# Kernel optimization log

Measured on AMD Instinct MI355X. Metric: run time of the kernel, lower is better.

## Reference

```python
import jax, jax.numpy as jnp
import numpy as np

D = 64  # d_model
NEG_INF = -1e9


def setup_inputs() -> dict:
    key = jax.random.key(0)
    ks = jax.random.split(key, 16)
    B, N = 16, 2048
    x = jax.random.normal(ks[0], (B, N, D), dtype=jnp.float32)
    adj = jax.random.randint(ks[1], (B, N, N), 0, 2, dtype=jnp.int32)
    s = 1.0 / np.sqrt(D)
    def lin(k, fan_in, fan_out):
        kw, kb = jax.random.split(k)
        W = jax.random.uniform(kw, (fan_in, fan_out), jnp.float32, -s, s)
        b = jax.random.uniform(kb, (fan_out,), jnp.float32, -s, s)
        return W, b
    Wq, bq = lin(ks[2], D, D)
    Wk, bk = lin(ks[3], D, D)
    Wv, bv = lin(ks[4], D, D)
    Wo, bo = lin(ks[5], D, D)
    sl = 1.0 / np.sqrt(2 * D)
    kw, kb = jax.random.split(ks[6])
    Wl = jax.random.uniform(kw, (2 * D, D), jnp.float32, -sl, sl)
    bl = jax.random.uniform(kb, (D,), jnp.float32, -sl, sl)
    return {"x": x, "adj": adj, "Wq": Wq, "bq": bq, "Wk": Wk, "bk": bk,
            "Wv": Wv, "bv": bv, "Wo": Wo, "bo": bo, "Wl": Wl, "bl": bl}


def reference(x, adj, Wq, bq, Wk, bk, Wv, bv, Wo, bo, Wl, bl):
    # single-head scaled dot-product attention masked by adjacency
    q = x @ Wq + bq          # [B,N,D]
    k = x @ Wk + bk          # [B,N,D]
    v = x @ Wv + bv          # [B,N,D]
    scores = jnp.einsum('bnd,bmd->bnm', q, k) / jnp.sqrt(jnp.float32(D))
    scores = jnp.where(adj > 0, scores, jnp.float32(NEG_INF))
    attn = jax.nn.softmax(scores, axis=-1)       # [B,N,N] graph-masked dist
    ctx = jnp.einsum('bnm,bmd->bnd', attn, v)
    ctx = ctx @ Wo + bo
    # concat residual input with attention output, project, ReLU
    y = jax.nn.relu(jnp.concatenate([x, ctx], axis=-1) @ Wl + bl)
    return (y, attn)
```

## Files before the change

### kernel.cpp

```cpp
#include <hip/hip_runtime.h>
#include <hip/hip_bf16.h>


#define NB 16
#define NN 2048
#define DI 64

using s8v  = __attribute__((ext_vector_type(8))) short;
using f32x4 = __attribute__((ext_vector_type(4))) float;

__device__ __forceinline__ ushort f2bf(float f) {
    __hip_bfloat16 h = __float2bfloat16(f);
    return *reinterpret_cast<ushort*>(&h);
}
__device__ __forceinline__ float bf2f(ushort u) {
    union { uint32_t u; float f; } v; v.u = ((uint32_t)u) << 16;
    return v.f;
}

__global__ __launch_bounds__(256)
void qkv_kernel(const float* __restrict__ x,
                const float* __restrict__ Wq, const float* __restrict__ bq,
                const float* __restrict__ Wk, const float* __restrict__ bk,
                const float* __restrict__ Wv, const float* __restrict__ bv,
                ushort* __restrict__ qh, ushort* __restrict__ ql,
                ushort* __restrict__ kh, ushort* __restrict__ kl,
                ushort* __restrict__ vt)
{
    __shared__ float xs[32 * 65];
    const int t  = threadIdx.x;
    const int r0 = blockIdx.x * 32;
    for (int idx = t; idx < 2048; idx += 256)
        xs[(idx >> 6) * 65 + (idx & 63)] = x[(size_t)r0 * 64 + idx];
    __syncthreads();

    const int col = t & 63;
    const int rg  = (t >> 6) * 8;

    float vacc[8];
    {
        float acc[8];
        #pragma unroll
        for (int i = 0; i < 8; ++i) acc[i] = bq[col];
        for (int d = 0; d < 64; ++d) {
            float w = Wq[d * 64 + col];
            #pragma unroll
            for (int i = 0; i < 8; ++i) acc[i] = fmaf(xs[(rg + i) * 65 + d], w, acc[i]);
        }
        #pragma unroll
        for (int i = 0; i < 8; ++i) {
            size_t o = (size_t)(r0 + rg + i) * 64 + col;
            ushort h = f2bf(acc[i]);
            qh[o] = h;
            ql[o] = f2bf(acc[i] - bf2f(h));
        }
    }
    {
        float acc[8];
        #pragma unroll
        for (int i = 0; i < 8; ++i) acc[i] = bk[col];
        for (int d = 0; d < 64; ++d) {
            float w = Wk[d * 64 + col];
            #pragma unroll
            for (int i = 0; i < 8; ++i) acc[i] = fmaf(xs[(rg + i) * 65 + d], w, acc[i]);
        }
        #pragma unroll
        for (int i = 0; i < 8; ++i) {
            size_t o = (size_t)(r0 + rg + i) * 64 + col;
            ushort h = f2bf(acc[i]);
            kh[o] = h;
            kl[o] = f2bf(acc[i] - bf2f(h));
        }
    }
    {
        #pragma unroll
        for (int i = 0; i < 8; ++i) vacc[i] = bv[col];
        for (int d = 0; d < 64; ++d) {
            float w = Wv[d * 64 + col];
            #pragma unroll
            for (int i = 0; i < 8; ++i) vacc[i] = fmaf(xs[(rg + i) * 65 + d], w, vacc[i]);
        }
    }
    __syncthreads();
    #pragma unroll
    for (int i = 0; i < 8; ++i) xs[(rg + i) * 65 + col] = vacc[i];
    __syncthreads();
    const int bb = r0 >> 11;
    const int n0 = r0 & 2047;
    for (int idx = t; idx < 2048; idx += 256) {
        int d = idx >> 5, j = idx & 31;
        vt[((size_t)bb * 64 + d) * 2048 + n0 + j] = f2bf(xs[j * 65 + d]);
    }
}

#define SP 2052

__global__ __launch_bounds__(512, 2)
void attn_kernel(const ushort* __restrict__ qh, const ushort* __restrict__ ql,
                 const ushort* __restrict__ kh, const ushort* __restrict__ kl,
                 const ushort* __restrict__ vt, const int* __restrict__ adj,
                 const float* __restrict__ x,
                 const float* __restrict__ Wo, const float* __restrict__ bo,
                 const float* __restrict__ Wl, const float* __restrict__ bl,
                 float* __restrict__ y, float* __restrict__ attn)
{
    __shared__ float S[16 * SP];
    __shared__ float red[512];
    __shared__ float mrow[16];
    __shared__ float rZ[16];
    __shared__ float cA[16][66];
    __shared__ float cB[16][66];
    __shared__ float cto[16][66];
    __shared__ float xs[16][64];

    const int t    = threadIdx.x;
    const int lane = t & 63;
    const int wave = t >> 6;
    const int b    = blockIdx.y;
    const int row0 = blockIdx.x * 16;

    const int la = lane & 15;
    const int ak = (lane >> 4) * 8;
    const int rb2 = (lane >> 4) * 4;

    const size_t qoff = ((size_t)(b * NN + row0) + la) * 64 + ak;
    const s8v aqh0 = *(const s8v*)(qh + qoff);
    const s8v aqh1 = *(const s8v*)(qh + qoff + 32);
    const s8v aql0 = *(const s8v*)(ql + qoff);
    const s8v aql1 = *(const s8v*)(ql + qoff + 32);

    const ushort* kph = kh + (size_t)b * NN * 64;
    const ushort* kpl = kl + (size_t)b * NN * 64;
    const int*    ap  = adj + ((size_t)b * NN + row0) * NN;

    for (int tile = 0; tile < 16; ++tile) {
        const int c = wave * 256 + tile * 16;
        const size_t ko = (size_t)(c + la) * 64 + ak;
        const s8v bh0 = *(const s8v*)(kph + ko);
        const s8v bh1 = *(const s8v*)(kph + ko + 32);
        const s8v bl0 = *(const s8v*)(kpl + ko);
        const s8v bl1 = *(const s8v*)(kpl + ko + 32);
        f32x4 acc = {0.f, 0.f, 0.f, 0.f};
        acc = __builtin_amdgcn_mfma_f32_16x16x32_bf16(aqh0, bh0, acc, 0, 0, 0);
        acc = __builtin_amdgcn_mfma_f32_16x16x32_bf16(aqh1, bh1, acc, 0, 0, 0);
        acc = __builtin_amdgcn_mfma_f32_16x16x32_bf16(aql0, bh0, acc, 0, 0, 0);
        acc = __builtin_amdgcn_mfma_f32_16x16x32_bf16(aql1, bh1, acc, 0, 0, 0);
        acc = __builtin_amdgcn_mfma_f32_16x16x32_bf16(aqh0, bl0, acc, 0, 0, 0);
        acc = __builtin_amdgcn_mfma_f32_16x16x32_bf16(aqh1, bl1, acc, 0, 0, 0);
        const int ccol = c + la;
        #pragma unroll
        for (int r = 0; r < 4; ++r) {
            int av = ap[(rb2 + r) * NN + ccol];
            S[(rb2 + r) * SP + ccol] = (av > 0) ? acc[r] * 0.125f : -1e9f;
        }
    }
    {
        const float* xp = x + (size_t)(b * NN + row0) * 64;
        for (int i2 = t; i2 < 1024; i2 += 512) xs[i2 >> 6][i2 & 63] = xp[i2];
    }
    __syncthreads();

    {
        const int r = t >> 5, i = t & 31;
        float m = -3.0e38f;
        for (int c2 = i; c2 < NN; c2 += 32) m = fmaxf(m, S[r * SP + c2]);
        red[t] = m;
        __syncthreads();
        if (t < 16) {
            float mm = red[t * 32];
            for (int j = 1; j < 32; ++j) mm = fmaxf(mm, red[t * 32 + j]);
            mrow[t] = mm;
        }
        __syncthreads();
        const float mm = mrow[r];
        float sum = 0.f;
        for (int c2 = i; c2 < NN; c2 += 32) {
            float e = __expf(S[r * SP + c2] - mm);
            S[r * SP + c2] = e;
            sum += e;
        }
        red[t] = sum;
        __syncthreads();
        if (t < 16) {
            float z = 0.f;
            for (int j = 0; j < 32; ++j) z += red[t * 32 + j];
            rZ[t] = 1.0f / z;
        }
        __syncthreads();
    }

    {
        float* aop = attn + ((size_t)b * NN + row0) * NN;
        for (int r = 0; r < 16; ++r) {
            const float rz = rZ[r];
            for (int c2 = t; c2 < NN; c2 += 512)
                aop[(size_t)r * NN + c2] = S[r * SP + c2] * rz;
        }
    }

    {
        const int half = wave >> 2;
        const int dt = (wave & 3) * 16;
        const ushort* vrow = vt + ((size_t)b * 64 + dt + la) * NN;
        f32x4 acc = {0.f, 0.f, 0.f, 0.f};
        const int kk0 = half * 1024;
        for (int kk = kk0; kk < kk0 + 1024; kk += 32) {
            const float* sp = &S[la * SP + kk + ak];
            s8v a;
            #pragma unroll
            for (int j = 0; j < 8; ++j) a[j] = (short)f2bf(sp[j]);
            const s8v bv8 = *(const s8v*)(vrow + kk + ak);
            acc = __builtin_amdgcn_mfma_f32_16x16x32_bf16(a, bv8, acc, 0, 0, 0);
        }
        float (*cbuf)[66] = half ? cB : cA;
        #pragma unroll
        for (int r = 0; r < 4; ++r) cbuf[rb2 + r][dt + la] = acc[r];
    }
    __syncthreads();

    for (int idx = t; idx < 1024; idx += 512) {
        const int r = idx >> 6, cg = idx & 63;
        const float rz = rZ[r];
        float a2 = bo[cg];
        for (int d = 0; d < 64; ++d) {
            float cv = (cA[r][d] + cB[r][d]) * rz;
            a2 = fmaf(cv, Wo[d * 64 + cg], a2);
        }
        cto[r][cg] = a2;
    }
    __syncthreads();

    {
        float* yp = y + (size_t)(b * NN + row0) * 64;
        for (int idx = t; idx < 1024; idx += 512) {
            const int r = idx >> 6, cg = idx & 63;
            float a2 = bl[cg];
            for (int d = 0; d < 64; ++d) a2 = fmaf(xs[r][d], Wl[d * 64 + cg], a2);
            for (int d = 0; d < 64; ++d) a2 = fmaf(cto[r][d], Wl[(64 + d) * 64 + cg], a2);
            yp[(size_t)r * 64 + cg] = fmaxf(a2, 0.f);
        }
    }
}

extern "C" void kernel_launch(void* const* d_in, const int* in_sizes, int n_in,
                              void* d_out, int out_size, void* d_ws, size_t ws_size,
                              hipStream_t stream) {
    const float* x  = (const float*)d_in[0];
    const int*   adj = (const int*)d_in[1];
    const float* Wq = (const float*)d_in[2];
    const float* bq = (const float*)d_in[3];
    const float* Wk = (const float*)d_in[4];
    const float* bk = (const float*)d_in[5];
    const float* Wv = (const float*)d_in[6];
    const float* bv = (const float*)d_in[7];
    const float* Wo = (const float*)d_in[8];
    const float* bo = (const float*)d_in[9];
    const float* Wl = (const float*)d_in[10];
    const float* bl = (const float*)d_in[11];

    float* y    = (float*)d_out;
    float* attn = (float*)d_out + (size_t)NB * NN * DI;

    const size_t QSZ = (size_t)NB * NN * DI;
    ushort* qh = (ushort*)d_ws;
    ushort* ql = qh + QSZ;
    ushort* kh = ql + QSZ;
    ushort* kl = kh + QSZ;
    ushort* vt = kl + QSZ;

    qkv_kernel<<<1024, 256, 0, stream>>>(x, Wq, bq, Wk, bk, Wv, bv, qh, ql, kh, kl, vt);
    attn_kernel<<<dim3(NN / 16, NB), 512, 0, stream>>>(qh, ql, kh, kl, vt, adj, x,
                                                       Wo, bo, Wl, bl, y, attn);
}
```

Measured before the change: 744.8 us.

## Keep masked scores in registers, store bf16 probabilities in LDS, remap blocks

The score tiles now stay in registers. Max and sum reductions are done with wave shuffles plus a small cross-wave buffer, which replaces the LDS-based row reductions. Exponentials are stored once as bf16 in shared memory, which halves LDS use, removes the float-to-bf16 conversion in the PV loop and allows vectorized attn writes. The grid is flattened and remapped so concurrent blocks span batches, and the x tile is read from global memory instead of being staged. The attn output is now rounded through bf16 before normalization, which adds precision error.

Result: faster. 709.7 us (-4.7%).

```diff
diff --git a/kernel.cpp b/kernel.cpp
--- a/kernel.cpp
+++ b/kernel.cpp
@@ -6,7 +6,7 @@
 #define NN 2048
 #define DI 64
 
-using s8v  = __attribute__((ext_vector_type(8))) short;
+using s8v   = __attribute__((ext_vector_type(8))) short;
 using f32x4 = __attribute__((ext_vector_type(4))) float;
 
 __device__ __forceinline__ ushort f2bf(float f) {
@@ -93,9 +93,9 @@
     }
 }
 
-#define SP 2052
-
-__global__ __launch_bounds__(512, 2)
+#define SP2 2056
+
+__global__ __launch_bounds__(512)
 void attn_kernel(const ushort* __restrict__ qh, const ushort* __restrict__ ql,
                  const ushort* __restrict__ kh, const ushort* __restrict__ kl,
                  const ushort* __restrict__ vt, const int* __restrict__ adj,
@@ -104,23 +104,26 @@
                  const float* __restrict__ Wl, const float* __restrict__ bl,
                  float* __restrict__ y, float* __restrict__ attn)
 {
-    __shared__ float S[16 * SP];
-    __shared__ float red[512];
-    __shared__ float mrow[16];
-    __shared__ float rZ[16];
+    __shared__ ushort S16[16 * SP2];
     __shared__ float cA[16][66];
     __shared__ float cB[16][66];
     __shared__ float cto[16][66];
-    __shared__ float xs[16][64];
+    __shared__ float mbuf[8][16];
+    __shared__ float zbuf[8][16];
+    __shared__ float mrow[16];
+    __shared__ float rZ[16];
 
     const int t    = threadIdx.x;
     const int lane = t & 63;
     const int wave = t >> 6;
-    const int b    = blockIdx.y;
-    const int row0 = blockIdx.x * 16;
-
-    const int la = lane & 15;
-    const int ak = (lane >> 4) * 8;
+
+    const int bid = blockIdx.x;
+    const int i0  = bid >> 3;
+    const int b   = (bid & 7) + 8 * (i0 >> 7);
+    const int row0 = (i0 & 127) * 16;
+
+    const int la  = lane & 15;
+    const int ak  = (lane >> 4) * 8;
     const int rb2 = (lane >> 4) * 4;
 
     const size_t qoff = ((size_t)(b * NN + row0) + la) * 64 + ak;
@@ -133,88 +136,120 @@
     const ushort* kpl = kl + (size_t)b * NN * 64;
     const int*    ap  = adj + ((size_t)b * NN + row0) * NN;
 
+    f32x4 acc[16];
+    int   adjv[16][4];
+    #pragma unroll
     for (int tile = 0; tile < 16; ++tile) {
         const int c = wave * 256 + tile * 16;
+        #pragma unroll
+        for (int r = 0; r < 4; ++r) adjv[tile][r] = ap[(rb2 + r) * NN + c + la];
         const size_t ko = (size_t)(c + la) * 64 + ak;
         const s8v bh0 = *(const s8v*)(kph + ko);
         const s8v bh1 = *(const s8v*)(kph + ko + 32);
         const s8v bl0 = *(const s8v*)(kpl + ko);
         const s8v bl1 = *(const s8v*)(kpl + ko + 32);
-        f32x4 acc = {0.f, 0.f, 0.f, 0.f};
-        acc = __builtin_amdgcn_mfma_f32_16x16x32_bf16(aqh0, bh0, acc, 0, 0, 0);
-        acc = __builtin_amdgcn_mfma_f32_16x16x32_bf16(aqh1, bh1, acc, 0, 0, 0);
-        acc = __builtin_amdgcn_mfma_f32_16x16x32_bf16(aql0, bh0, acc, 0, 0, 0);
-        acc = __builtin_amdgcn_mfma_f32_16x16x32_bf16(aql1, bh1, acc, 0, 0, 0);
-        acc = __builtin_amdgcn_mfma_f32_16x16x32_bf16(aqh0, bl0, acc, 0, 0, 0);
-        acc = __builtin_amdgcn_mfma_f32_16x16x32_bf16(aqh1, bl1, acc, 0, 0, 0);
-        const int ccol = c + la;
+        f32x4 a = {0.f, 0.f, 0.f, 0.f};
+        a = __builtin_amdgcn_mfma_f32_16x16x32_bf16(aqh0, bh0, a, 0, 0, 0);
+        a = __builtin_amdgcn_mfma_f32_16x16x32_bf16(aqh1, bh1, a, 0, 0, 0);
+        a = __builtin_amdgcn_mfma_f32_16x16x32_bf16(aql0, bh0, a, 0, 0, 0);
+        a = __builtin_amdgcn_mfma_f32_16x16x32_bf16(aql1, bh1, a, 0, 0, 0);
+        a = __builtin_amdgcn_mfma_f32_16x16x32_bf16(aqh0, bl0, a, 0, 0, 0);
+        a = __builtin_amdgcn_mfma_f32_16x16x32_bf16(aqh1, bl1, a, 0, 0, 0);
+        acc[tile] = a;
+    }
+    #pragma unroll
+    for (int tile = 0; tile < 16; ++tile) {
+        #pragma unroll
+        for (int r = 0; r < 4; ++r)
+            acc[tile][r] = (adjv[tile][r] > 0) ? acc[tile][r] * 0.125f : -1e9f;
+    }
+
+    float vm[4];
+    #pragma unroll
+    for (int r = 0; r < 4; ++r) {
+        float m = acc[0][r];
+        #pragma unroll
+        for (int tile = 1; tile < 16; ++tile) m = fmaxf(m, acc[tile][r]);
+        vm[r] = m;
+    }
+    #pragma unroll
+    for (int off = 1; off < 16; off <<= 1) {
+        #pragma unroll
+        for (int r = 0; r < 4; ++r) vm[r] = fmaxf(vm[r], __shfl_xor(vm[r], off));
+    }
+    if (la == 0) {
+        #pragma unroll
+        for (int r = 0; r < 4; ++r) mbuf[wave][rb2 + r] = vm[r];
+    }
+    __syncthreads();
+    if (t < 16) {
+        float m = mbuf[0][t];
+        #pragma unroll
+        for (int w = 1; w < 8; ++w) m = fmaxf(m, mbuf[w][t]);
+        mrow[t] = m;
+    }
+    __syncthreads();
+
+    float gm[4], vs[4];
+    #pragma unroll
+    for (int r = 0; r < 4; ++r) { gm[r] = mrow[rb2 + r]; vs[r] = 0.f; }
+    #pragma unroll
+    for (int tile = 0; tile < 16; ++tile) {
+        const int c = wave * 256 + tile * 16;
         #pragma unroll
         for (int r = 0; r < 4; ++r) {
-            int av = ap[(rb2 + r) * NN + ccol];
-            S[(rb2 + r) * SP + ccol] = (av > 0) ? acc[r] * 0.125f : -1e9f;
-        }
-    }
-    {
-        const float* xp = x + (size_t)(b * NN + row0) * 64;
-        for (int i2 = t; i2 < 1024; i2 += 512) xs[i2 >> 6][i2 & 63] = xp[i2];
-    }
-    __syncthreads();
-
-    {
-        const int r = t >> 5, i = t & 31;
-        float m = -3.0e38f;
-        for (int c2 = i; c2 < NN; c2 += 32) m = fmaxf(m, S[r * SP + c2]);
-        red[t] = m;
-        __syncthreads();
-        if (t < 16) {
-            float mm = red[t * 32];
-            for (int j = 1; j < 32; ++j) mm = fmaxf(mm, red[t * 32 + j]);
-            mrow[t] = mm;
-        }
-        __syncthreads();
-        const float mm = mrow[r];
-        float sum = 0.f;
-        for (int c2 = i; c2 < NN; c2 += 32) {
-            float e = __expf(S[r * SP + c2] - mm);
-            S[r * SP + c2] = e;
-            sum += e;
-        }
-        red[t] = sum;
-        __syncthreads();
-        if (t < 16) {
-            float z = 0.f;
-            for (int j = 0; j < 32; ++j) z += red[t * 32 + j];
-            rZ[t] = 1.0f / z;
-        }
-        __syncthreads();
-    }
+            float e = __expf(acc[tile][r] - gm[r]);
+            vs[r] += e;
+            S16[(rb2 + r) * SP2 + c + la] = f2bf(e);
+        }
+    }
+    #pragma unroll
+    for (int off = 1; off < 16; off <<= 1) {
+        #pragma unroll
+        for (int r = 0; r < 4; ++r) vs[r] += __shfl_xor(vs[r], off);
+    }
+    if (la == 0) {
+        #pragma unroll
+        for (int r = 0; r < 4; ++r) zbuf[wave][rb2 + r] = vs[r];
+    }
+    __syncthreads();
+    if (t < 16) {
+        float z = 0.f;
+        #pragma unroll
+        for (int w = 0; w < 8; ++w) z += zbuf[w][t];
+        rZ[t] = 1.0f / z;
+    }
+    __syncthreads();
 
     {
         float* aop = attn + ((size_t)b * NN + row0) * NN;
         for (int r = 0; r < 16; ++r) {
             const float rz = rZ[r];
-            for (int c2 = t; c2 < NN; c2 += 512)
-                aop[(size_t)r * NN + c2] = S[r * SP + c2] * rz;
+            const uint2 u = *(const uint2*)(&S16[r * SP2 + 4 * t]);
+            float4 o;
+            o.x = bf2f((ushort)(u.x))       * rz;
+            o.y = bf2f((ushort)(u.x >> 16)) * rz;
+            o.z = bf2f((ushort)(u.y))       * rz;
+            o.w = bf2f((ushort)(u.y >> 16)) * rz;
+            *(float4*)(aop + (size_t)r * NN + 4 * t) = o;
         }
     }
 
     {
         const int half = wave >> 2;
-        const int dt = (wave & 3) * 16;
+        const int dt   = (wave & 3) * 16;
         const ushort* vrow = vt + ((size_t)b * 64 + dt + la) * NN;
-        f32x4 acc = {0.f, 0.f, 0.f, 0.f};
+        f32x4 a = {0.f, 0.f, 0.f, 0.f};
         const int kk0 = half * 1024;
+        #pragma unroll 4
         for (int kk = kk0; kk < kk0 + 1024; kk += 32) {
-            const float* sp = &S[la * SP + kk + ak];
-            s8v a;
-            #pragma unroll
-            for (int j = 0; j < 8; ++j) a[j] = (short)f2bf(sp[j]);
+            const s8v pa  = *(const s8v*)(&S16[la * SP2 + kk + ak]);
             const s8v bv8 = *(const s8v*)(vrow + kk + ak);
-            acc = __builtin_amdgcn_mfma_f32_16x16x32_bf16(a, bv8, acc, 0, 0, 0);
+            a = __builtin_amdgcn_mfma_f32_16x16x32_bf16(pa, bv8, a, 0, 0, 0);
         }
         float (*cbuf)[66] = half ? cB : cA;
         #pragma unroll
-        for (int r = 0; r < 4; ++r) cbuf[rb2 + r][dt + la] = acc[r];
+        for (int r = 0; r < 4; ++r) cbuf[rb2 + r][dt + la] = a[r];
     }
     __syncthreads();
 
@@ -231,11 +266,12 @@
     __syncthreads();
 
     {
-        float* yp = y + (size_t)(b * NN + row0) * 64;
+        const float* xp = x + (size_t)(b * NN + row0) * 64;
+        float*       yp = y + (size_t)(b * NN + row0) * 64;
         for (int idx = t; idx < 1024; idx += 512) {
             const int r = idx >> 6, cg = idx & 63;
             float a2 = bl[cg];
-            for (int d = 0; d < 64; ++d) a2 = fmaf(xs[r][d], Wl[d * 64 + cg], a2);
+            for (int d = 0; d < 64; ++d) a2 = fmaf(xp[r * 64 + d], Wl[d * 64 + cg], a2);
             for (int d = 0; d < 64; ++d) a2 = fmaf(cto[r][d], Wl[(64 + d) * 64 + cg], a2);
             yp[(size_t)r * 64 + cg] = fmaxf(a2, 0.f);
         }
@@ -269,6 +305,6 @@
     ushort* vt = kl + QSZ;
 
     qkv_kernel<<<1024, 256, 0, stream>>>(x, Wq, bq, Wk, bk, Wv, bv, qh, ql, kh, kl, vt);
-    attn_kernel<<<dim3(NN / 16, NB), 512, 0, stream>>>(qh, ql, kh, kl, vt, adj, x,
-                                                       Wo, bo, Wl, bl, y, attn);
-}
+    attn_kernel<<<NB * (NN / 16), 512, 0, stream>>>(qh, ql, kh, kl, vt, adj, x,
+                                                    Wo, bo, Wl, bl, y, attn);
+}
```
